# Kernel optimization log

Hardware: AMD Instinct MI355X
Metric: run time of the kernel (lower is better)

The kernel has to match this reference:

```python
import jax, jax.numpy as jnp
import numpy as np

KS = 3
STRIDE = 1
PADDING = 1
P_SCALE = 10.0
Q_SCALE = 100.0
EPS = 1e-12


def unfold2d(x):
    # x: [N, C, H, W] -> patches [N, C, Hout, Wout, KS*KS]
    x = jnp.pad(x, ((0, 0), (0, 0), (PADDING, PADDING), (PADDING, PADDING)))
    n, c, h, w = x.shape
    hout = (h - KS) // STRIDE + 1
    wout = (w - KS) // STRIDE + 1
    shifts = []
    for a in range(KS):
        for b in range(KS):
            shifts.append(x[:, :, a:a + hout * STRIDE:STRIDE, b:b + wout * STRIDE:STRIDE])
    return jnp.stack(shifts, axis=-1)  # l = a*KS + b, matching flatten of (a, b)


def setup_inputs() -> dict:
    key = jax.random.key(0)
    k1, k2 = jax.random.split(key)
    x = jax.random.normal(k1, (16, 64, 64, 64), dtype=jnp.float32)
    # xavier_uniform for weights [out_c, in_c, k*k]: fan_in=64, fan_out=9 per torch semantics on 3D
    fan_in, fan_out = 64, 9
    limit = float(np.sqrt(6.0 / (fan_in + fan_out)))
    weights = jax.random.uniform(k2, (128, 64, 9), dtype=jnp.float32, minval=-limit, maxval=limit)
    p = jnp.full((128,), float(2 ** 0.5) * P_SCALE, dtype=jnp.float32)
    q = jnp.full((1,), 10.0, dtype=jnp.float32)
    return {"x": x, "weights": weights, "p": p, "q": q}


def reference(x, weights, p, q):
    patches = unfold2d(x)  # [N, C, H, W, L]
    qn = q / Q_SCALE
    scale = jnp.square(qn)  # scalar (shape [1])
    # norm over (C, L) for patches; over (C, L) for weights
    x_norm = jnp.sqrt(jnp.sum(jnp.square(patches), axis=(1, 4), keepdims=True) + EPS) + scale
    w_norm = jnp.sqrt(jnp.sum(jnp.square(weights), axis=(1, 2), keepdims=True) + EPS) + scale
    y = jnp.einsum('nchwl,vcl->nvhw', patches / x_norm, weights / w_norm)
    sign = jnp.sign(y)
    expo = jnp.square(p / P_SCALE)[None, :, None, None]
    return sign * jnp.power(jnp.abs(y) + EPS, expo)
```

## Files before the change

### kernel.cpp

```cpp
#include <hip/hip_runtime.h>
#include <math.h>
#include <stdint.h>

#define EPS 1e-12f

typedef __attribute__((ext_vector_type(8))) short short8v;
typedef __attribute__((ext_vector_type(8))) unsigned short us8;
typedef __attribute__((ext_vector_type(4))) float f32x4;

__device__ __forceinline__ unsigned short f2bf(float f) {
  union { float f; uint32_t u; } c; c.f = f;
  uint32_t u = c.u;
  uint32_t r = (u + 0x7FFFu + ((u >> 16) & 1u)) >> 16;
  return (unsigned short)r;
}

__device__ __forceinline__ void gl_lds16(const void* g, void* l) {
  __builtin_amdgcn_global_load_lds(
      (const __attribute__((address_space(1))) unsigned int*)g,
      (__attribute__((address_space(3))) unsigned int*)l, 16, 0, 0);
}


__global__ __launch_bounds__(256) void prep_all(
    const float* __restrict__ x, const float* __restrict__ w,
    const float* __restrict__ q, unsigned short* __restrict__ xT,
    unsigned short* __restrict__ Wb, float* __restrict__ s) {
  __shared__ float tile[64][65];
  int b = blockIdx.x;
  int tid = threadIdx.x;

  if (b >= 1024) {
    int v = (b - 1024) * 4 + (tid >> 6);
    int c = tid & 63;
    float qn = q[0] * 0.01f;
    float scale = qn * qn;
    const float* wp = w + (v * 64 + c) * 9;
    float vals[9];
    float ss = 0.f;
#pragma unroll
    for (int j = 0; j < 9; ++j) { vals[j] = wp[j]; ss += vals[j] * vals[j]; }
#pragma unroll
    for (int off = 32; off > 0; off >>= 1) ss += __shfl_xor(ss, off);
    float inv = 1.0f / (sqrtf(ss + EPS) + scale);
    int pos = (((c >> 3) ^ (v & 7)) << 3) | (c & 7);
#pragma unroll
    for (int j = 0; j < 9; ++j) Wb[(j * 128 + v) * 64 + pos] = f2bf(vals[j] * inv);
    return;
  }

  int n = b >> 6, h = b & 63;
  int c = tid >> 2, qq = tid & 3;
  const float* xp = x + ((size_t)(n * 64 + c)) * 4096 + h * 64;
#pragma unroll
  for (int k = 0; k < 4; ++k) {
    int w0 = qq * 16 + k * 4;
    float4 v4 = *(const float4*)(xp + w0);
    tile[c][w0 + 0] = v4.x; tile[c][w0 + 1] = v4.y;
    tile[c][w0 + 2] = v4.z; tile[c][w0 + 3] = v4.w;
  }
  __syncthreads();
  int ww = tid >> 2;
  float ss = 0.f;
  unsigned short* orow = xT + ((size_t)(n * 4096 + h * 64 + ww)) * 64;
#pragma unroll
  for (int t = 0; t < 2; ++t) {
    int slot = qq * 2 + t;
    int lc = slot ^ (ww & 7);
    us8 st;
#pragma unroll
    for (int e = 0; e < 8; ++e) {
      float f = tile[lc * 8 + e][ww];
      ss += f * f;
      st[e] = f2bf(f);
    }
    *(us8*)(orow + slot * 8) = st;
  }
  ss += __shfl_xor(ss, 1);
  ss += __shfl_xor(ss, 2);
  if (qq == 0) s[n * 4096 + h * 64 + ww] = ss;
}

__global__ __launch_bounds__(256, 2) void conv_mfma(
    const unsigned short* __restrict__ xT, const unsigned short* __restrict__ Wb,
    const float* __restrict__ s, const float* __restrict__ p,
    const float* __restrict__ q, float* __restrict__ out) {
  __shared__ unsigned short xs[4 * 66 * 64];
  __shared__ unsigned short wl[2 * 128 * 64];
  __shared__ float xiv[2 * 64];

  int b = blockIdx.x;
  int n = b >> 5, hg = b & 31;
  int h0 = hg * 2;
  int tid = threadIdx.x;
  int lane = tid & 63, wid = tid >> 6;
  int wv = wid & 1, wp = wid >> 1;
  int lp = lane & 15, lg = lane >> 4;

  auto stage_w = [&](int bufi, int l) {
    const unsigned short* src = Wb + l * 8192 + wid * 2048;
    unsigned short* dst = wl + bufi * 8192 + wid * 2048;
#pragma unroll
    for (int i = 0; i < 4; ++i)
      gl_lds16(src + i * 512 + lane * 8, dst + i * 512);
  };
  stage_w(0, 0);

  {
    int hh = h0 - 1 + wid;
    unsigned short* dst = xs + wid * 4224 + 64;
    if ((unsigned)hh < 64u) {
      const unsigned short* src = xT + ((size_t)(n * 4096 + hh * 64)) * 64;
#pragma unroll
      for (int i = 0; i < 8; ++i)
        gl_lds16(src + i * 512 + lane * 8, dst + i * 512);
    } else {
      us8 z = {};
#pragma unroll
      for (int i = 0; i < 8; ++i)
        *(us8*)(dst + i * 512 + lane * 8) = z;
    }
  }
  if (tid < 64) {
    int row = tid >> 4, side = (tid >> 3) & 1, j = tid & 7;
    us8 z = {};
    *(us8*)(xs + row * 4224 + (side ? 65 : 0) * 64 + j * 8) = z;
  }
  if (tid < 128) {
    int r = tid >> 6, ww = tid & 63;
    int h = h0 + r;
    float qn = q[0] * 0.01f;
    float scale = qn * qn;
    const float* sp = s + n * 4096;
    float a = 0.f;
#pragma unroll
    for (int dh = -1; dh <= 1; ++dh) {
      int hh = h + dh;
      if ((unsigned)hh < 64u) {
#pragma unroll
        for (int dw = -1; dw <= 1; ++dw) {
          int w2 = ww + dw;
          if ((unsigned)w2 < 64u) a += sp[hh * 64 + w2];
        }
      }
    }
    xiv[r * 64 + ww] = 1.0f / (sqrtf(a + EPS) + scale);
  }

  f32x4 acc[4][4];
#pragma unroll
  for (int i = 0; i < 4; ++i)
#pragma unroll
    for (int j = 0; j < 4; ++j) acc[i][j] = (f32x4){0.f, 0.f, 0.f, 0.f};

  __syncthreads();

  int buf = 0;
#pragma unroll
  for (int l = 0; l < 9; ++l) {
    if (l < 8) stage_w(buf ^ 1, l + 1);
    const int a = l / 3, bs = l % 3;
    const unsigned short* xrow = xs + (wp + a) * 4224;
    const unsigned short* wbase = wl + buf * 8192 + wv * 4096;
#pragma unroll
    for (int half = 0; half < 2; ++half) {
      const int cbase = half * 4;
      short8v av[4], bv[4];
#pragma unroll
      for (int vg = 0; vg < 4; ++vg)
        av[vg] = *(const short8v*)(wbase + (vg * 16 + lp) * 64 +
                                   ((cbase + lg) ^ (lp & 7)) * 8);
#pragma unroll
      for (int pg = 0; pg < 4; ++pg) {
        int wx = pg * 16 + lp + bs - 1;
        bv[pg] = *(const short8v*)(xrow + (wx + 1) * 64 +
                                   ((cbase + lg) ^ (wx & 7)) * 8);
      }
#pragma unroll
      for (int pg = 0; pg < 4; ++pg)
#pragma unroll
        for (int vg = 0; vg < 4; ++vg)
          acc[pg][vg] = __builtin_amdgcn_mfma_f32_16x16x32_bf16(
              bv[pg], av[vg], acc[pg][vg], 0, 0, 0);
    }
    if (l < 8) {
      __syncthreads();
      buf ^= 1;
    }
  }

  int h = h0 + wp;
#pragma unroll
  for (int vg = 0; vg < 4; ++vg) {
    int v = wv * 64 + vg * 16 + lp;
    float t0 = p[v] * 0.1f;
    float e = t0 * t0;
    float* ob = out + ((size_t)(n * 128 + v)) * 4096 + h * 64;
#pragma unroll
    for (int pg = 0; pg < 4; ++pg) {
      int w4 = pg * 16 + lg * 4;
      float4 xv = *(const float4*)&xiv[wp * 64 + w4];
      float yv[4] = {acc[pg][vg][0] * xv.x, acc[pg][vg][1] * xv.y,
                     acc[pg][vg][2] * xv.z, acc[pg][vg][3] * xv.w};
      f32x4 o;
#pragma unroll
      for (int r = 0; r < 4; ++r) {
        float y = yv[r];
        float t = fabsf(y) + EPS;
        float rv = exp2f(e * log2f(t));
        o[r] = (y == 0.0f) ? 0.0f : copysignf(rv, y);
      }
      *(f32x4*)(ob + w4) = o;
    }
  }
}

extern "C" void kernel_launch(void* const* d_in, const int* in_sizes, int n_in,
                              void* d_out, int out_size, void* d_ws, size_t ws_size,
                              hipStream_t stream) {
  const float* x = (const float*)d_in[0];
  const float* w = (const float*)d_in[1];
  const float* p = (const float*)d_in[2];
  const float* q = (const float*)d_in[3];
  float* out = (float*)d_out;

  char* wsb = (char*)d_ws;
  unsigned short* xT = (unsigned short*)(wsb);
  unsigned short* Wb = (unsigned short*)(wsb + 8388608);
  float* s = (float*)(wsb + 8536064);

  prep_all<<<1056, 256, 0, stream>>>(x, w, q, xT, Wb, s);
  conv_mfma<<<512, 256, 0, stream>>>(xT, Wb, s, p, q, out);
}
```

Before: 33.73 us.

## Compute patch norms in conv kernel and single-buffer weights via registers

The prep kernel is restructured so each block handles 8 channels by 8 rows, packing one 8-channel slot per pixel, and it no longer writes per-pixel sum-of-squares. The conv kernel now computes squared norms from the bf16 tiles already staged in LDS, which removes the workspace array and its global reads. Weight staging changes from double-buffered async global-to-LDS copies to register prefetch plus a single LDS buffer, and launch bounds rise to 3 blocks per CU. This cuts LDS use and global traffic but adds an extra barrier per tap and computes norms from bf16-rounded values, which slightly changes accuracy.

```diff
diff --git a/kernel.cpp b/kernel.cpp
--- a/kernel.cpp
+++ b/kernel.cpp
@@ -15,6 +15,11 @@
   return (unsigned short)r;
 }
 
+__device__ __forceinline__ float bf2f(unsigned short v) {
+  union { uint32_t u; float f; } c; c.u = ((uint32_t)v) << 16;
+  return c.f;
+}
+
 __device__ __forceinline__ void gl_lds16(const void* g, void* l) {
   __builtin_amdgcn_global_load_lds(
       (const __attribute__((address_space(1))) unsigned int*)g,
@@ -25,8 +30,8 @@
 __global__ __launch_bounds__(256) void prep_all(
     const float* __restrict__ x, const float* __restrict__ w,
     const float* __restrict__ q, unsigned short* __restrict__ xT,
-    unsigned short* __restrict__ Wb, float* __restrict__ s) {
-  __shared__ float tile[64][65];
+    unsigned short* __restrict__ Wb) {
+  __shared__ float raw[8 * 512];
   int b = blockIdx.x;
   int tid = threadIdx.x;
 
@@ -49,44 +54,33 @@
     return;
   }
 
-  int n = b >> 6, h = b & 63;
-  int c = tid >> 2, qq = tid & 3;
-  const float* xp = x + ((size_t)(n * 64 + c)) * 4096 + h * 64;
-#pragma unroll
-  for (int k = 0; k < 4; ++k) {
-    int w0 = qq * 16 + k * 4;
-    float4 v4 = *(const float4*)(xp + w0);
-    tile[c][w0 + 0] = v4.x; tile[c][w0 + 1] = v4.y;
-    tile[c][w0 + 2] = v4.z; tile[c][w0 + 3] = v4.w;
-  }
+  int n = b >> 6, cc = (b >> 3) & 7, hb = b & 7;
+  int e = tid >> 5, i = tid & 31;
+  const float* src = x + ((size_t)(n * 64 + cc * 8 + e)) * 4096 + hb * 512 + i * 16;
+  float* dst = raw + e * 512 + i * 16;
+#pragma unroll
+  for (int k = 0; k < 4; ++k)
+    *(float4*)(dst + 4 * k) = *(const float4*)(src + 4 * k);
   __syncthreads();
-  int ww = tid >> 2;
-  float ss = 0.f;
-  unsigned short* orow = xT + ((size_t)(n * 4096 + h * 64 + ww)) * 64;
-#pragma unroll
-  for (int t = 0; t < 2; ++t) {
-    int slot = qq * 2 + t;
-    int lc = slot ^ (ww & 7);
-    us8 st;
-#pragma unroll
-    for (int e = 0; e < 8; ++e) {
-      float f = tile[lc * 8 + e][ww];
-      ss += f * f;
-      st[e] = f2bf(f);
-    }
-    *(us8*)(orow + slot * 8) = st;
-  }
-  ss += __shfl_xor(ss, 1);
-  ss += __shfl_xor(ss, 2);
-  if (qq == 0) s[n * 4096 + h * 64 + ww] = ss;
-}
-
-__global__ __launch_bounds__(256, 2) void conv_mfma(
+#pragma unroll
+  for (int t2 = 0; t2 < 2; ++t2) {
+    int pix = t2 * 256 + tid;
+    int r = pix >> 6, ww = pix & 63;
+    us8 pk;
+#pragma unroll
+    for (int e2 = 0; e2 < 8; ++e2) pk[e2] = f2bf(raw[e2 * 512 + r * 64 + ww]);
+    int slot = cc ^ (ww & 7);
+    *(us8*)(xT + ((size_t)(n * 4096 + (hb * 8 + r) * 64 + ww)) * 64 + slot * 8) = pk;
+  }
+}
+
+__global__ __launch_bounds__(256, 3) void conv_mfma(
     const unsigned short* __restrict__ xT, const unsigned short* __restrict__ Wb,
-    const float* __restrict__ s, const float* __restrict__ p,
-    const float* __restrict__ q, float* __restrict__ out) {
+    const float* __restrict__ p, const float* __restrict__ q,
+    float* __restrict__ out) {
   __shared__ unsigned short xs[4 * 66 * 64];
-  __shared__ unsigned short wl[2 * 128 * 64];
+  __shared__ unsigned short wl[128 * 64];
+  __shared__ float sf[4 * 64];
   __shared__ float xiv[2 * 64];
 
   int b = blockIdx.x;
@@ -97,14 +91,15 @@
   int wv = wid & 1, wp = wid >> 1;
   int lp = lane & 15, lg = lane >> 4;
 
-  auto stage_w = [&](int bufi, int l) {
-    const unsigned short* src = Wb + l * 8192 + wid * 2048;
-    unsigned short* dst = wl + bufi * 8192 + wid * 2048;
-#pragma unroll
-    for (int i = 0; i < 4; ++i)
-      gl_lds16(src + i * 512 + lane * 8, dst + i * 512);
-  };
-  stage_w(0, 0);
+  const us8* wsrc = (const us8*)Wb + tid;
+  us8* wl8 = (us8*)wl;
+  {
+    us8 w0[4];
+#pragma unroll
+    for (int k = 0; k < 4; ++k) w0[k] = wsrc[k * 256];
+#pragma unroll
+    for (int k = 0; k < 4; ++k) wl8[tid + k * 256] = w0[k];
+  }
 
   {
     int hh = h0 - 1 + wid;
@@ -126,23 +121,33 @@
     us8 z = {};
     *(us8*)(xs + row * 4224 + (side ? 65 : 0) * 64 + j * 8) = z;
   }
+  __syncthreads();
+
+  {
+    int r = tid >> 6, ww = tid & 63;
+    const unsigned short* px = xs + r * 4224 + (ww + 1) * 64;
+    float ss = 0.f;
+#pragma unroll
+    for (int j = 0; j < 8; ++j) {
+      us8 v = *(const us8*)(px + ((j ^ (ww & 7)) * 8));
+#pragma unroll
+      for (int e = 0; e < 8; ++e) { float f = bf2f(v[e]); ss += f * f; }
+    }
+    sf[r * 64 + ww] = ss;
+  }
+  __syncthreads();
+
   if (tid < 128) {
     int r = tid >> 6, ww = tid & 63;
-    int h = h0 + r;
     float qn = q[0] * 0.01f;
     float scale = qn * qn;
-    const float* sp = s + n * 4096;
     float a = 0.f;
 #pragma unroll
-    for (int dh = -1; dh <= 1; ++dh) {
-      int hh = h + dh;
-      if ((unsigned)hh < 64u) {
-#pragma unroll
-        for (int dw = -1; dw <= 1; ++dw) {
-          int w2 = ww + dw;
-          if ((unsigned)w2 < 64u) a += sp[hh * 64 + w2];
-        }
-      }
+    for (int dr = 0; dr < 3; ++dr) {
+      const float* base = sf + (r + dr) * 64;
+      a += base[ww];
+      if (ww > 0) a += base[ww - 1];
+      if (ww < 63) a += base[ww + 1];
     }
     xiv[r * 64 + ww] = 1.0f / (sqrtf(a + EPS) + scale);
   }
@@ -153,15 +158,16 @@
 #pragma unroll
     for (int j = 0; j < 4; ++j) acc[i][j] = (f32x4){0.f, 0.f, 0.f, 0.f};
 
-  __syncthreads();
-
-  int buf = 0;
 #pragma unroll
   for (int l = 0; l < 9; ++l) {
-    if (l < 8) stage_w(buf ^ 1, l + 1);
+    us8 nw[4];
+    if (l < 8) {
+#pragma unroll
+      for (int k = 0; k < 4; ++k) nw[k] = wsrc[(l + 1) * 1024 + k * 256];
+    }
     const int a = l / 3, bs = l % 3;
     const unsigned short* xrow = xs + (wp + a) * 4224;
-    const unsigned short* wbase = wl + buf * 8192 + wv * 4096;
+    const unsigned short* wbase = wl + wv * 4096;
 #pragma unroll
     for (int half = 0; half < 2; ++half) {
       const int cbase = half * 4;
@@ -185,7 +191,9 @@
     }
     if (l < 8) {
       __syncthreads();
-      buf ^= 1;
+#pragma unroll
+      for (int k = 0; k < 4; ++k) wl8[tid + k * 256] = nw[k];
+      __syncthreads();
     }
   }
 
@@ -227,8 +235,7 @@
   char* wsb = (char*)d_ws;
   unsigned short* xT = (unsigned short*)(wsb);
   unsigned short* Wb = (unsigned short*)(wsb + 8388608);
-  float* s = (float*)(wsb + 8536064);
-
-  prep_all<<<1056, 256, 0, stream>>>(x, w, q, xT, Wb, s);
-  conv_mfma<<<512, 256, 0, stream>>>(xT, Wb, s, p, q, out);
-}
+
+  prep_all<<<1056, 256, 0, stream>>>(x, w, q, xT, Wb);
+  conv_mfma<<<512, 256, 0, stream>>>(xT, Wb, p, q, out);
+}
```

After: 39.45 us. 17.0% more time.
